# Kernel optimization log

Hardware: AMD Instinct MI355X
Metric: run time of the kernel (lower is better)

## Reference

```python
import jax, jax.numpy as jnp
import numpy as np
import math

D_MODEL = 512
N_HEADS = 8
C = 1

def setup_inputs() -> dict:
    key = jax.random.key(0)
    ks = jax.random.split(key, 7)
    B, L, D = 4, 2048, 512
    f = lambda k, s: jax.random.normal(k, s, dtype=jnp.float32)
    return {
        "queries": f(ks[0], (B, L, D)),
        "keys": f(ks[1], (B, L, D)),
        "values": f(ks[2], (B, L, D)),
        "wq": f(ks[3], (D, D_MODEL)) * (1.0 / math.sqrt(D)),
        "wk": f(ks[4], (D, D_MODEL)) * (1.0 / math.sqrt(D)),
        "wv": f(ks[5], (D, D_MODEL)) * (1.0 / math.sqrt(D)),
        "wo": f(ks[6], (D_MODEL, D_MODEL)) * (1.0 / math.sqrt(D_MODEL)),
    }

def reference(queries, keys, values, wq, wk, wv, wo):
    B, Lq, _ = queries.shape
    Lk = keys.shape[1]
    H = N_HEADS
    Dh = D_MODEL // N_HEADS
    # projections -> [B,H,L,Dh]
    Q = (queries @ wq).reshape(B, Lq, H, Dh).transpose(0, 2, 1, 3)
    K = (keys @ wk).reshape(B, Lk, H, Dh).transpose(0, 2, 1, 3)
    V = (values @ wv).reshape(B, Lk, H, Dh).transpose(0, 2, 1, 3)
    # NOTE: original computes rfft/irfft correlation then OVERWRITES it with
    # this dense einsum; FFT branch is dead code and omitted here.
    corr = jnp.einsum('bhid,bhjd->bhij', Q, K)  # [B,H,Lq,Lk]
    # k derived from values.shape[3] == d_head in the original (quirk preserved)
    k = max(1, min(int(C * math.log(Dh)), Dh))
    mean_corr = corr.mean(axis=(1, 2))  # [B, Lk]
    top_vals, top_idx = jax.lax.top_k(mean_corr, k)  # [B,k]
    w = jax.nn.softmax(top_vals, axis=-1)  # [B,k]
    # rolled[b,j,h,l,d] = V[b,h,(l + delay[b,j]) % Lk, d]  (tf.roll with shift=-delay)
    idx = (jnp.arange(Lk)[None, None, :] + top_idx[:, :, None]) % Lk  # [B,k,Lk]
    gathered = jnp.take_along_axis(V[:, None], idx[:, :, None, :, None], axis=3)  # [B,k,H,Lk,Dh]
    agg = jnp.einsum('bk,bkhld->bhld', w, gathered)  # [B,H,Lk,Dh]
    # original: transpose (0,3,1,2) then reshape -> [B, Lq, d_model]
    out = agg.transpose(0, 3, 1, 2).reshape(B, Lq, D_MODEL)
    return out @ wo
```

## Files before the change

### kernel.cpp

```cpp
#include <hip/hip_runtime.h>
#include <hip/hip_bf16.h>
#include <float.h>
#include <math.h>

#define B  4
#define L  2048
#define D  512
#define K4 4

typedef __attribute__((ext_vector_type(8))) short  bf16x8;
typedef __attribute__((ext_vector_type(4))) float  f32x4;

#define VMIXB_OFF  0u
#define TT_OFF     8388608u
#define WVT_OFF    16777216u
#define WOT_OFF    17301504u
#define QPART_OFF  17825792u
#define TPART_OFF  18350080u
#define U_OFF      18415616u
#define SC_OFF     18423808u
#define W_OFF      18456576u
#define I_OFF      18456640u

static __device__ __forceinline__ unsigned short f2b(float f) {
    __hip_bfloat16 h = __float2bfloat16(f);
    return *reinterpret_cast<unsigned short*>(&h);
}

__global__ void k_qpart(const float* __restrict__ q, float* __restrict__ qpart) {
    int b = blockIdx.x, lc = blockIdx.y;
    int c4 = threadIdx.x & 127, half = threadIdx.x >> 7;
    const float4* p = (const float4*)q + ((size_t)b * L + lc * 64 + half * 32) * 128 + c4;
    float4 a = make_float4(0.f, 0.f, 0.f, 0.f);
#pragma unroll 8
    for (int l = 0; l < 32; ++l) {
        float4 x = p[(size_t)l * 128];
        a.x += x.x; a.y += x.y; a.z += x.z; a.w += x.w;
    }
    ((float4*)qpart)[((b * 64) + lc * 2 + half) * 128 + c4] = a;
}

__global__ void k_wt(const float* __restrict__ wv, const float* __restrict__ wo,
                     unsigned short* __restrict__ wvT, unsigned short* __restrict__ woT) {
    __shared__ float s[32][33];
    const float* src = (blockIdx.z == 0) ? wv : wo;
    unsigned short* dst = (blockIdx.z == 0) ? wvT : woT;
    int c0 = blockIdx.x * 32, n0 = blockIdx.y * 32;
    int tid = threadIdx.x, col = tid & 31, r8 = tid >> 5;
#pragma unroll
    for (int rr = 0; rr < 4; ++rr) {
        int r = rr * 8 + r8;
        s[r][col] = src[(size_t)(c0 + r) * D + n0 + col];
    }
    __syncthreads();
#pragma unroll
    for (int rr = 0; rr < 4; ++rr) {
        int r = rr * 8 + r8;
        dst[(size_t)(n0 + r) * D + c0 + col] = f2b(s[col][r]);
    }
}

__global__ void k_tpart(const float* __restrict__ wq, const float* __restrict__ qpart,
                        float* __restrict__ tpart) {
    __shared__ float part[256];
    __shared__ float qs[64];
    int b = blockIdx.x, jc = blockIdx.y, tid = threadIdx.x;
    int jj = tid & 63, cg = tid >> 6;
    float p = 0.f;
#pragma unroll
    for (int c = cg * 16; c < cg * 16 + 16; ++c)
        p += qpart[((b * 64) + c) * D + jc * 64 + jj];
    part[tid] = p;
    __syncthreads();
    if (tid < 64) qs[tid] = part[tid] + part[tid + 64] + part[tid + 128] + part[tid + 192];
    __syncthreads();
    float a0 = 0.f, a1 = 0.f;
#pragma unroll 8
    for (int j = 0; j < 64; ++j) {
        const float* wr = wq + (size_t)(jc * 64 + j) * D;
        float qv = qs[j];
        a0 += wr[tid] * qv;
        a1 += wr[tid + 256] * qv;
    }
    tpart[((b * 8) + jc) * D + tid] = a0;
    tpart[((b * 8) + jc) * D + tid + 256] = a1;
}

__global__ void k_uvec(const float* __restrict__ wk, const float* __restrict__ tpart,
                       float* __restrict__ u) {
    __shared__ __align__(16) float ts[D];
    int b = blockIdx.x, tid = threadIdx.x;
    for (int d = tid; d < D; d += 256) {
        float s = 0.f;
#pragma unroll
        for (int c = 0; c < 8; ++c) s += tpart[((b * 8) + c) * D + d];
        ts[d] = s;
    }
    __syncthreads();
    int wave = tid >> 6, lane = tid & 63;
    const float4* wk4 = (const float4*)wk;
    float4 t0 = *(const float4*)&ts[lane * 4];
    float4 t1 = *(const float4*)&ts[256 + lane * 4];
#pragma unroll
    for (int rr = 0; rr < 4; ++rr) {
        int i = blockIdx.y * 16 + wave * 4 + rr;
        float4 w0 = wk4[(size_t)i * 128 + lane];
        float4 w1 = wk4[(size_t)i * 128 + 64 + lane];
        float acc = w0.x * t0.x + w0.y * t0.y + w0.z * t0.z + w0.w * t0.w
                  + w1.x * t1.x + w1.y * t1.y + w1.z * t1.z + w1.w * t1.w;
        for (int m = 32; m; m >>= 1) acc += __shfl_xor(acc, m, 64);
        if (lane == 0) u[b * D + i] = acc * (1.f / 16384.f);
    }
}

__global__ void k_scores(const float* __restrict__ keys, const float* __restrict__ u,
                         float* __restrict__ sc) {
    __shared__ __align__(16) float us[D];
    int b = blockIdx.x, tid = threadIdx.x;
    for (int d = tid; d < D; d += 256) us[d] = u[b * D + d];
    __syncthreads();
    int wave = tid >> 6, lane = tid & 63;
    int j = blockIdx.y * 4 + wave;
    const float4* kp = (const float4*)(keys + ((size_t)b * L + j) * D);
    float4 u0 = *(const float4*)&us[lane * 4];
    float4 u1 = *(const float4*)&us[256 + lane * 4];
    float4 x0 = kp[lane], x1 = kp[lane + 64];
    float acc = x0.x * u0.x + x0.y * u0.y + x0.z * u0.z + x0.w * u0.w
              + x1.x * u1.x + x1.y * u1.y + x1.z * u1.z + x1.w * u1.w;
    for (int m = 32; m; m >>= 1) acc += __shfl_xor(acc, m, 64);
    if (lane == 0) sc[b * L + j] = acc;
}

__global__ void k_top4(const float* __restrict__ sc, float* __restrict__ wout,
                       int* __restrict__ iout) {
    __shared__ float sv[L];
    __shared__ float wv4[4];
    __shared__ int wi4[4];
    __shared__ float topv[K4];
    __shared__ int topi[K4];
    int b = blockIdx.x, tid = threadIdx.x;
    int wave = tid >> 6, lane = tid & 63;
    for (int i = tid; i < L; i += 256) sv[i] = sc[b * L + i];
    __syncthreads();
    for (int it = 0; it < K4; ++it) {
        float bv = -FLT_MAX;
        int bi = 0x7fffffff;
#pragma unroll
        for (int i = 0; i < 8; ++i) {
            int idx = tid + i * 256;
            float v = sv[idx];
            if (v > bv) { bv = v; bi = idx; }
        }
        for (int m = 32; m; m >>= 1) {
            float v2 = __shfl_xor(bv, m, 64);
            int i2 = __shfl_xor(bi, m, 64);
            if (v2 > bv || (v2 == bv && i2 < bi)) { bv = v2; bi = i2; }
        }
        if (lane == 0) { wv4[wave] = bv; wi4[wave] = bi; }
        __syncthreads();
        if (tid == 0) {
            float mv = wv4[0]; int mi = wi4[0];
            for (int w = 1; w < 4; ++w)
                if (wv4[w] > mv || (wv4[w] == mv && wi4[w] < mi)) { mv = wv4[w]; mi = wi4[w]; }
            topv[it] = mv; topi[it] = mi; sv[mi] = -FLT_MAX;
        }
        __syncthreads();
    }
    if (tid == 0) {
        float mx = topv[0];
        for (int i = 1; i < K4; ++i) mx = fmaxf(mx, topv[i]);
        float ssum = 0.f, e[K4];
        for (int i = 0; i < K4; ++i) { e[i] = expf(topv[i] - mx); ssum += e[i]; }
        for (int i = 0; i < K4; ++i) { wout[b * K4 + i] = e[i] / ssum; iout[b * K4 + i] = topi[i]; }
    }
}

__global__ void k_vmixb(const float* __restrict__ values, const float* __restrict__ wb,
                        const int* __restrict__ ib, uint4* __restrict__ vmixb) {
    __shared__ float wsh[K4];
    __shared__ int ish[K4];
    size_t t = (size_t)blockIdx.x * 256 + threadIdx.x;
    int b = (int)(t >> 17);
    if (threadIdx.x < K4) { wsh[threadIdx.x] = wb[b * K4 + threadIdx.x]; ish[threadIdx.x] = ib[b * K4 + threadIdx.x]; }
    __syncthreads();
    int l  = (int)((t >> 6) & (L - 1));
    int g8 = (int)(t & 63);
    const float4* vp = (const float4*)values;
    float4 r0 = make_float4(0.f, 0.f, 0.f, 0.f), r1 = r0;
#pragma unroll
    for (int j = 0; j < K4; ++j) {
        int ls = (l + ish[j]) & (L - 1);
        const float4* p = vp + ((size_t)b * L + ls) * 128 + g8 * 2;
        float4 x0 = p[0], x1 = p[1];
        float w = wsh[j];
        r0.x += w * x0.x; r0.y += w * x0.y; r0.z += w * x0.z; r0.w += w * x0.w;
        r1.x += w * x1.x; r1.y += w * x1.y; r1.z += w * x1.z; r1.w += w * x1.w;
    }
    uint4 o;
    o.x = (unsigned)f2b(r0.x) | ((unsigned)f2b(r0.y) << 16);
    o.y = (unsigned)f2b(r0.z) | ((unsigned)f2b(r0.w) << 16);
    o.z = (unsigned)f2b(r1.x) | ((unsigned)f2b(r1.y) << 16);
    o.w = (unsigned)f2b(r1.z) | ((unsigned)f2b(r1.w) << 16);
    vmixb[t] = o;
}

__global__ __launch_bounds__(256) void k_gemm1(const unsigned short* __restrict__ A,
                                               const unsigned short* __restrict__ Bt,
                                               unsigned short* __restrict__ Tt) {
    __shared__ __align__(16) unsigned short As[2][128][40];
    __shared__ __align__(16) unsigned short Bs[2][64][40];
    int m0 = blockIdx.x * 128, n0 = blockIdx.y * 64;
    int tid = threadIdx.x;
    int wave = tid >> 6, lane = tid & 63;
    int wr = wave >> 1, wc = wave & 1;
    int lr = lane & 15, lg = lane >> 4;
    f32x4 acc[4][2];
#pragma unroll
    for (int i = 0; i < 4; ++i)
#pragma unroll
        for (int j = 0; j < 2; ++j) acc[i][j] = (f32x4){0.f, 0.f, 0.f, 0.f};

    int aR = tid >> 1, aC = (tid & 1) * 16;
    int bR = tid >> 2, bC = (tid & 3) * 8;
    const unsigned short* Ap = A + (size_t)(m0 + aR) * D + aC;
    const unsigned short* Bp = Bt + (size_t)(n0 + bR) * D + bC;
    {
        uint4 va0 = *(const uint4*)(Ap);
        uint4 va1 = *(const uint4*)(Ap + 8);
        uint4 vb  = *(const uint4*)(Bp);
        *(uint4*)&As[0][aR][aC]     = va0;
        *(uint4*)&As[0][aR][aC + 8] = va1;
        *(uint4*)&Bs[0][bR][bC]     = vb;
    }
    __syncthreads();
    int cur = 0;
    for (int t = 0; t < 15; ++t) {
        int k0 = (t + 1) * 32;
        uint4 va0 = *(const uint4*)(Ap + k0);
        uint4 va1 = *(const uint4*)(Ap + k0 + 8);
        uint4 vb  = *(const uint4*)(Bp + k0);
        bf16x8 a[4], bq[2];
#pragma unroll
        for (int i = 0; i < 4; ++i) a[i] = *(const bf16x8*)&As[cur][wr * 64 + i * 16 + lr][lg * 8];
#pragma unroll
        for (int j = 0; j < 2; ++j) bq[j] = *(const bf16x8*)&Bs[cur][wc * 32 + j * 16 + lr][lg * 8];
#pragma unroll
        for (int i = 0; i < 4; ++i)
#pragma unroll
            for (int j = 0; j < 2; ++j)
                acc[i][j] = __builtin_amdgcn_mfma_f32_16x16x32_bf16(a[i], bq[j], acc[i][j], 0, 0, 0);
        *(uint4*)&As[cur ^ 1][aR][aC]     = va0;
        *(uint4*)&As[cur ^ 1][aR][aC + 8] = va1;
        *(uint4*)&Bs[cur ^ 1][bR][bC]     = vb;
        __syncthreads();
        cur ^= 1;
    }
    {
        bf16x8 a[4], bq[2];
#pragma unroll
        for (int i = 0; i < 4; ++i) a[i] = *(const bf16x8*)&As[cur][wr * 64 + i * 16 + lr][lg * 8];
#pragma unroll
        for (int j = 0; j < 2; ++j) bq[j] = *(const bf16x8*)&Bs[cur][wc * 32 + j * 16 + lr][lg * 8];
#pragma unroll
        for (int i = 0; i < 4; ++i)
#pragma unroll
            for (int j = 0; j < 2; ++j)
                acc[i][j] = __builtin_amdgcn_mfma_f32_16x16x32_bf16(a[i], bq[j], acc[i][j], 0, 0, 0);
    }
    int bb = m0 >> 11;
    int lbase = (m0 & (L - 1)) + wr * 64 + lg * 4;
#pragma unroll
    for (int i = 0; i < 4; ++i) {
        int lp = lbase + i * 16;
#pragma unroll
        for (int j = 0; j < 2; ++j) {
            int cn = n0 + wc * 32 + j * 16 + lr;
            uint2 pk;
            pk.x = (unsigned)f2b(acc[i][j][0]) | ((unsigned)f2b(acc[i][j][1]) << 16);
            pk.y = (unsigned)f2b(acc[i][j][2]) | ((unsigned)f2b(acc[i][j][3]) << 16);
            *(uint2*)&Tt[((size_t)bb * D + cn) * L + lp] = pk;
        }
    }
}

__global__ __launch_bounds__(256) void k_gemm2(const unsigned short* __restrict__ Tt,
                                               const unsigned short* __restrict__ Bt,
                                               float* __restrict__ out) {
    __shared__ __align__(16) unsigned short As[2][128][40];
    __shared__ __align__(16) unsigned short Bs[2][64][40];
    int m0 = blockIdx.x * 128, n0 = blockIdx.y * 64;
    int bs = blockIdx.z;
    int bb = bs >> 2, s = bs & 3;
    const unsigned short* Ab = Tt + (size_t)bb * D * L + (size_t)s * 512;
    int tid = threadIdx.x;
    int wave = tid >> 6, lane = tid & 63;
    int wr = wave >> 1, wc = wave & 1;
    int lr = lane & 15, lg = lane >> 4;
    f32x4 acc[4][2];
#pragma unroll
    for (int i = 0; i < 4; ++i)
#pragma unroll
        for (int j = 0; j < 2; ++j) acc[i][j] = (f32x4){0.f, 0.f, 0.f, 0.f};

    int aR = tid >> 1, aC = (tid & 1) * 16;
    int bR = tid >> 2, bC = (tid & 3) * 8;
    const unsigned short* Ap = Ab + (size_t)(m0 + aR) * L + aC;
    const unsigned short* Bp = Bt + (size_t)(n0 + bR) * D + bC;
    {
        uint4 va0 = *(const uint4*)(Ap);
        uint4 va1 = *(const uint4*)(Ap + 8);
        uint4 vb  = *(const uint4*)(Bp);
        *(uint4*)&As[0][aR][aC]     = va0;
        *(uint4*)&As[0][aR][aC + 8] = va1;
        *(uint4*)&Bs[0][bR][bC]     = vb;
    }
    __syncthreads();
    int cur = 0;
    for (int t = 0; t < 15; ++t) {
        int k0 = (t + 1) * 32;
        uint4 va0 = *(const uint4*)(Ap + k0);
        uint4 va1 = *(const uint4*)(Ap + k0 + 8);
        uint4 vb  = *(const uint4*)(Bp + k0);
        bf16x8 a[4], bq[2];
#pragma unroll
        for (int i = 0; i < 4; ++i) a[i] = *(const bf16x8*)&As[cur][wr * 64 + i * 16 + lr][lg * 8];
#pragma unroll
        for (int j = 0; j < 2; ++j) bq[j] = *(const bf16x8*)&Bs[cur][wc * 32 + j * 16 + lr][lg * 8];
#pragma unroll
        for (int i = 0; i < 4; ++i)
#pragma unroll
            for (int j = 0; j < 2; ++j)
                acc[i][j] = __builtin_amdgcn_mfma_f32_16x16x32_bf16(a[i], bq[j], acc[i][j], 0, 0, 0);
        *(uint4*)&As[cur ^ 1][aR][aC]     = va0;
        *(uint4*)&As[cur ^ 1][aR][aC + 8] = va1;
        *(uint4*)&Bs[cur ^ 1][bR][bC]     = vb;
        __syncthreads();
        cur ^= 1;
    }
    {
        bf16x8 a[4], bq[2];
#pragma unroll
        for (int i = 0; i < 4; ++i) a[i] = *(const bf16x8*)&As[cur][wr * 64 + i * 16 + lr][lg * 8];
#pragma unroll
        for (int j = 0; j < 2; ++j) bq[j] = *(const bf16x8*)&Bs[cur][wc * 32 + j * 16 + lr][lg * 8];
#pragma unroll
        for (int i = 0; i < 4; ++i)
#pragma unroll
            for (int j = 0; j < 2; ++j)
                acc[i][j] = __builtin_amdgcn_mfma_f32_16x16x32_bf16(a[i], bq[j], acc[i][j], 0, 0, 0);
    }
#pragma unroll
    for (int i = 0; i < 4; ++i) {
#pragma unroll
        for (int j = 0; j < 2; ++j) {
            int n = n0 + wc * 32 + j * 16 + lr;
#pragma unroll
            for (int r = 0; r < 4; ++r) {
                int m = m0 + wr * 64 + i * 16 + lg * 4 + r;
                int rr = ((m & 63) << 5) | ((m >> 6) << 2) | s;
                out[((size_t)bb * L + rr) * D + n] = acc[i][j][r];
            }
        }
    }
}

extern "C" void kernel_launch(void* const* d_in, const int* in_sizes, int n_in,
                              void* d_out, int out_size, void* d_ws, size_t ws_size,
                              hipStream_t stream) {
    const float* queries = (const float*)d_in[0];
    const float* keys    = (const float*)d_in[1];
    const float* values  = (const float*)d_in[2];
    const float* wq      = (const float*)d_in[3];
    const float* wk      = (const float*)d_in[4];
    const float* wv      = (const float*)d_in[5];
    const float* wo      = (const float*)d_in[6];
    float* out = (float*)d_out;
    char* ws = (char*)d_ws;

    unsigned short* vmixb = (unsigned short*)(ws + VMIXB_OFF);
    unsigned short* Tt    = (unsigned short*)(ws + TT_OFF);
    unsigned short* wvT   = (unsigned short*)(ws + WVT_OFF);
    unsigned short* woT   = (unsigned short*)(ws + WOT_OFF);
    float* qpart = (float*)(ws + QPART_OFF);
    float* tpart = (float*)(ws + TPART_OFF);
    float* u     = (float*)(ws + U_OFF);
    float* sc    = (float*)(ws + SC_OFF);
    float* wbuf  = (float*)(ws + W_OFF);
    int*   ibuf  = (int*)(ws + I_OFF);

    k_qpart<<<dim3(B, 32), 256, 0, stream>>>(queries, qpart);
    k_wt<<<dim3(16, 16, 2), 256, 0, stream>>>(wv, wo, wvT, woT);
    k_tpart<<<dim3(B, 8), 256, 0, stream>>>(wq, qpart, tpart);
    k_uvec<<<dim3(B, 32), 256, 0, stream>>>(wk, tpart, u);
    k_scores<<<dim3(B, 512), 256, 0, stream>>>(keys, u, sc);
    k_top4<<<B, 256, 0, stream>>>(sc, wbuf, ibuf);
    k_vmixb<<<2048, 256, 0, stream>>>(values, wbuf, ibuf, (uint4*)vmixb);
    k_gemm1<<<dim3(64, 8), 256, 0, stream>>>(vmixb, wvT, Tt);
    k_gemm2<<<dim3(4, 8, 16), 256, 0, stream>>>(Tt, woT, out);
}
```

Before: 70.39 us.

## Fuse qpart with weight transpose and top-k selection into vmix kernel

Merges the query-partial-sum and weight-transpose kernels into one launch split by block index. It also folds the top-4 selection and softmax into the value-mixing kernel, so every one of the 2048 blocks recomputes top-k for its batch from the scores. This removes two kernel launches and the small intermediate weight/index buffers. The cost is redundant top-k work per block: 2048 blocks each load 8KB of scores and run four reduction rounds with barriers.

```diff
diff --git a/kernel.cpp b/kernel.cpp
--- a/kernel.cpp
+++ b/kernel.cpp
@@ -19,44 +19,49 @@
 #define TPART_OFF  18350080u
 #define U_OFF      18415616u
 #define SC_OFF     18423808u
-#define W_OFF      18456576u
-#define I_OFF      18456640u
 
 static __device__ __forceinline__ unsigned short f2b(float f) {
     __hip_bfloat16 h = __float2bfloat16(f);
     return *reinterpret_cast<unsigned short*>(&h);
 }
 
-__global__ void k_qpart(const float* __restrict__ q, float* __restrict__ qpart) {
-    int b = blockIdx.x, lc = blockIdx.y;
-    int c4 = threadIdx.x & 127, half = threadIdx.x >> 7;
-    const float4* p = (const float4*)q + ((size_t)b * L + lc * 64 + half * 32) * 128 + c4;
-    float4 a = make_float4(0.f, 0.f, 0.f, 0.f);
+__global__ __launch_bounds__(256) void k_prep1(const float* __restrict__ q,
+                                               const float* __restrict__ wv, const float* __restrict__ wo,
+                                               float* __restrict__ qpart,
+                                               unsigned short* __restrict__ wvT, unsigned short* __restrict__ woT) {
+    __shared__ float s[32][33];
+    int bid = blockIdx.x, tid = threadIdx.x;
+    if (bid < 128) {
+        int b = bid >> 5, lc = bid & 31;
+        int c4 = tid & 127, half = tid >> 7;
+        const float4* p = (const float4*)q + ((size_t)b * L + lc * 64 + half * 32) * 128 + c4;
+        float4 a = make_float4(0.f, 0.f, 0.f, 0.f);
 #pragma unroll 8
-    for (int l = 0; l < 32; ++l) {
-        float4 x = p[(size_t)l * 128];
-        a.x += x.x; a.y += x.y; a.z += x.z; a.w += x.w;
-    }
-    ((float4*)qpart)[((b * 64) + lc * 2 + half) * 128 + c4] = a;
-}
-
-__global__ void k_wt(const float* __restrict__ wv, const float* __restrict__ wo,
-                     unsigned short* __restrict__ wvT, unsigned short* __restrict__ woT) {
-    __shared__ float s[32][33];
-    const float* src = (blockIdx.z == 0) ? wv : wo;
-    unsigned short* dst = (blockIdx.z == 0) ? wvT : woT;
-    int c0 = blockIdx.x * 32, n0 = blockIdx.y * 32;
-    int tid = threadIdx.x, col = tid & 31, r8 = tid >> 5;
-#pragma unroll
-    for (int rr = 0; rr < 4; ++rr) {
-        int r = rr * 8 + r8;
-        s[r][col] = src[(size_t)(c0 + r) * D + n0 + col];
-    }
-    __syncthreads();
-#pragma unroll
-    for (int rr = 0; rr < 4; ++rr) {
-        int r = rr * 8 + r8;
-        dst[(size_t)(n0 + r) * D + c0 + col] = f2b(s[col][r]);
+        for (int l = 0; l < 32; ++l) {
+            float4 x = p[(size_t)l * 128];
+            a.x += x.x; a.y += x.y; a.z += x.z; a.w += x.w;
+        }
+        ((float4*)qpart)[((b * 64) + lc * 2 + half) * 128 + c4] = a;
+    } else {
+        int id2 = bid - 128;
+        int c0 = (id2 >> 4) * 32, n0 = (id2 & 15) * 32;
+        int col = tid & 31, r8 = tid >> 5;
+        for (int z = 0; z < 2; ++z) {
+            const float* src = z ? wo : wv;
+            unsigned short* dst = z ? woT : wvT;
+#pragma unroll
+            for (int rr = 0; rr < 4; ++rr) {
+                int r = rr * 8 + r8;
+                s[r][col] = src[(size_t)(c0 + r) * D + n0 + col];
+            }
+            __syncthreads();
+#pragma unroll
+            for (int rr = 0; rr < 4; ++rr) {
+                int r = rr * 8 + r8;
+                dst[(size_t)(n0 + r) * D + c0 + col] = f2b(s[col][r]);
+            }
+            __syncthreads();
+        }
     }
 }
 
@@ -131,17 +136,18 @@
     if (lane == 0) sc[b * L + j] = acc;
 }
 
-__global__ void k_top4(const float* __restrict__ sc, float* __restrict__ wout,
-                       int* __restrict__ iout) {
+__global__ __launch_bounds__(256) void k_vmixb(const float* __restrict__ values,
+                                               const float* __restrict__ sc,
+                                               uint4* __restrict__ vmixb) {
     __shared__ float sv[L];
-    __shared__ float wv4[4];
-    __shared__ int wi4[4];
-    __shared__ float topv[K4];
-    __shared__ int topi[K4];
-    int b = blockIdx.x, tid = threadIdx.x;
-    int wave = tid >> 6, lane = tid & 63;
+    __shared__ float wv4[4]; __shared__ int wi4[4];
+    __shared__ float wsh[K4]; __shared__ int ish[K4];
+    int tid = threadIdx.x;
+    int wave = tid >> 6, lane = tid & 63;
+    int b = (int)(blockIdx.x >> 9);
     for (int i = tid; i < L; i += 256) sv[i] = sc[b * L + i];
     __syncthreads();
+    float topv[K4]; int topi[K4];
     for (int it = 0; it < K4; ++it) {
         float bv = -FLT_MAX;
         int bi = 0x7fffffff;
@@ -158,31 +164,27 @@
         }
         if (lane == 0) { wv4[wave] = bv; wi4[wave] = bi; }
         __syncthreads();
-        if (tid == 0) {
-            float mv = wv4[0]; int mi = wi4[0];
-            for (int w = 1; w < 4; ++w)
-                if (wv4[w] > mv || (wv4[w] == mv && wi4[w] < mi)) { mv = wv4[w]; mi = wi4[w]; }
-            topv[it] = mv; topi[it] = mi; sv[mi] = -FLT_MAX;
-        }
+        float mv = wv4[0]; int mi = wi4[0];
+#pragma unroll
+        for (int w = 1; w < 4; ++w)
+            if (wv4[w] > mv || (wv4[w] == mv && wi4[w] < mi)) { mv = wv4[w]; mi = wi4[w]; }
+        topv[it] = mv; topi[it] = mi;
+        if (tid == 0) sv[mi] = -FLT_MAX;
         __syncthreads();
     }
     if (tid == 0) {
         float mx = topv[0];
+#pragma unroll
         for (int i = 1; i < K4; ++i) mx = fmaxf(mx, topv[i]);
         float ssum = 0.f, e[K4];
+#pragma unroll
         for (int i = 0; i < K4; ++i) { e[i] = expf(topv[i] - mx); ssum += e[i]; }
-        for (int i = 0; i < K4; ++i) { wout[b * K4 + i] = e[i] / ssum; iout[b * K4 + i] = topi[i]; }
-    }
-}
-
-__global__ void k_vmixb(const float* __restrict__ values, const float* __restrict__ wb,
-                        const int* __restrict__ ib, uint4* __restrict__ vmixb) {
-    __shared__ float wsh[K4];
-    __shared__ int ish[K4];
-    size_t t = (size_t)blockIdx.x * 256 + threadIdx.x;
-    int b = (int)(t >> 17);
-    if (threadIdx.x < K4) { wsh[threadIdx.x] = wb[b * K4 + threadIdx.x]; ish[threadIdx.x] = ib[b * K4 + threadIdx.x]; }
-    __syncthreads();
+#pragma unroll
+        for (int i = 0; i < K4; ++i) { wsh[i] = e[i] / ssum; ish[i] = topi[i]; }
+    }
+    __syncthreads();
+
+    size_t t = (size_t)blockIdx.x * 256 + tid;
     int l  = (int)((t >> 6) & (L - 1));
     int g8 = (int)(t & 63);
     const float4* vp = (const float4*)values;
@@ -385,16 +387,12 @@
     float* tpart = (float*)(ws + TPART_OFF);
     float* u     = (float*)(ws + U_OFF);
     float* sc    = (float*)(ws + SC_OFF);
-    float* wbuf  = (float*)(ws + W_OFF);
-    int*   ibuf  = (int*)(ws + I_OFF);
-
-    k_qpart<<<dim3(B, 32), 256, 0, stream>>>(queries, qpart);
-    k_wt<<<dim3(16, 16, 2), 256, 0, stream>>>(wv, wo, wvT, woT);
+
+    k_prep1<<<384, 256, 0, stream>>>(queries, wv, wo, qpart, wvT, woT);
     k_tpart<<<dim3(B, 8), 256, 0, stream>>>(wq, qpart, tpart);
     k_uvec<<<dim3(B, 32), 256, 0, stream>>>(wk, tpart, u);
     k_scores<<<dim3(B, 512), 256, 0, stream>>>(keys, u, sc);
-    k_top4<<<B, 256, 0, stream>>>(sc, wbuf, ibuf);
-    k_vmixb<<<2048, 256, 0, stream>>>(values, wbuf, ibuf, (uint4*)vmixb);
+    k_vmixb<<<2048, 256, 0, stream>>>(values, sc, (uint4*)vmixb);
     k_gemm1<<<dim3(64, 8), 256, 0, stream>>>(vmixb, wvT, Tt);
     k_gemm2<<<dim3(4, 8, 16), 256, 0, stream>>>(Tt, woT, out);
 }
```

Result: faster. 67.22 us (-4.5%).
